# Performance work log

Hardware: AMD Instinct MI355X
Metric: run time of the kernel (lower is better)

Reference implementation:

```python
import jax, jax.numpy as jnp
import numpy as np

N_STROKES = 512
H = 256
W = 256
EPS = 1e-6


def setup_inputs() -> dict:
    key = jax.random.key(0)
    k1, k2, k3, k4, k5, k6 = jax.random.split(key, 6)
    canvas = jnp.zeros((3, H, W), dtype=jnp.float32)
    target = jax.random.uniform(k1, (3, H, W), dtype=jnp.float32)
    offset = jax.random.normal(k2, (N_STROKES, 2, 1), dtype=jnp.float32) * 0.5 + 0.5
    sigma = jax.random.uniform(k3, (N_STROKES, 2, 1), dtype=jnp.float32) * 0.5 + 0.2
    theta = jax.random.uniform(k4, (N_STROKES, 1), dtype=jnp.float32) * (2.0 * np.pi)
    color = jax.random.uniform(k5, (N_STROKES, 3, 1, 1), dtype=jnp.float32)
    alpha = jax.random.normal(k6, (N_STROKES, 1, 1, 1), dtype=jnp.float32) * 0.1
    return {"canvas": canvas, "target": target, "offset": offset,
            "sigma": sigma, "theta": theta, "color": color, "alpha": alpha}


def reference(canvas, target, offset, sigma, theta, color, alpha):
    h, w = canvas.shape[-2:]
    ratio = w / h  # width_to_height_ratio

    # normalized pixel grid, matching torch.linspace(0, w-1, w)/w
    ws = jnp.arange(w, dtype=jnp.float32) / w
    hs = jnp.arange(h, dtype=jnp.float32) / h
    x, y = jnp.meshgrid(ws, hs, indexing="xy")          # (H, W) each
    coords = jnp.stack([x, y], axis=0).reshape(1, 2, -1)  # (1, 2, H*W)
    coords = coords - offset                              # (n, 2, H*W)

    # rotation matrix per stroke: [[cos, -sin], [sin, -cos]] (as in source)
    cos_t = jnp.cos(theta)
    sin_t = jnp.sin(theta)
    rot = jnp.concatenate([cos_t, -sin_t, sin_t, -cos_t], axis=-1).reshape(-1, 2, 2)
    coords = jnp.einsum("nij,njp->nip", rot, coords)      # (n, 2, H*W)

    # aspect-corrected sigma (only for the gaussian field, not the loss)
    sig = jnp.concatenate([sigma[:, :1] / ratio, sigma[:, 1:]], axis=1)  # (n, 2, 1)

    quad = jnp.sum(jnp.square(coords) / (2.0 * jnp.square(sig)), axis=1)  # (n, H*W)
    pdf = jnp.exp(-quad)
    maxes = jnp.max(pdf, axis=-1, keepdims=True)          # per-stroke max-normalize
    pdf = pdf / (maxes + EPS)

    strokes = pdf.reshape(-1, 1, h, w) * alpha * color    # (n, 3, H, W)
    out = jax.nn.sigmoid(canvas + jnp.sum(strokes, axis=0))

    # loss_fn(out, target)
    l2 = jnp.mean(jnp.square(out - target))
    sharpness = jnp.mean(jnp.abs(1.0 - sigma[:, 0] / sigma[:, 1])) * 0.001
    transparency = -jnp.mean(jnp.abs(alpha)) * 0.001
    mse = jnp.mean(jnp.square(target - out))
    psnr = 10.0 * jnp.log10(1.0 / (mse + 1e-12))
    loss = l2 + transparency + sharpness - psnr / 30.0
    return out, loss
```

## Files before the change

kernel.cpp:

```cpp
#include <hip/hip_runtime.h>
#include <hip/hip_bf16.h>

#define HH 256
#define WW 256
#define NPIX (HH*WW)
#define NS 512

#define A_P  0
#define A_Q  1
#define A_T1 2
#define A_R  3
#define A_S  4
#define A_T2 5
#define A_C0 6
#define A_C1 7
#define A_C2 8
#define A_SH 9
#define A_TR 10
#define L2_SLOT  (11*NS)
#define CNT_SLOT (11*NS + 1)

#define TEAMS 8
#define SPT   (NS/TEAMS)
#define PPT   4
#define BLK   512
#define K2_GRID 256

#define L2E 1.4426950408889634f

#if __has_builtin(__builtin_amdgcn_exp2f)
#define EXP2F(x) __builtin_amdgcn_exp2f(x)
#else
#define EXP2F(x) exp2f(x)
#endif
#if __has_builtin(__builtin_amdgcn_rcpf)
#define RCPF(x) __builtin_amdgcn_rcpf(x)
#else
#define RCPF(x) (1.0f/(x))
#endif

__global__ __launch_bounds__(256) void k1_prep(
    const float* __restrict__ offset, const float* __restrict__ sigma,
    const float* __restrict__ theta,  const float* __restrict__ color,
    const float* __restrict__ alpha,  float* __restrict__ wsf)
{
    const int n = blockIdx.x;
    const int i = threadIdx.x;

    const float ox = offset[2*n], oy = offset[2*n+1];
    const float s0 = sigma[2*n],  s1 = sigma[2*n+1];
    const float th = theta[n];

    const float kk = sqrtf(0.5f * L2E);
    const float ra = kk / s0;
    const float rb = kk / s1;

    float s, c;
    __sincosf(th, &s, &c);
    const float P = ra * c,  Q = -ra * s,  T1 = ra * (-c * ox + s * oy);
    const float R = rb * s,  S = -rb * c,  T2 = rb * (-s * ox + c * oy);

    const float y     = (float)i / (float)HH;
    const float beta  = fmaf(Q, y, T1);
    const float delta = fmaf(S, y, T2);
    const float A     = P * P + R * R;
    const float xstar = -(P * beta + R * delta) / A;
    int j0 = (int)floorf(xstar * (float)WW);
    j0 = max(0, min(WW - 1, j0));
    const int j1 = min(WW - 1, j0 + 1);
    const float x0 = (float)j0 / (float)WW, x1 = (float)j1 / (float)WW;
    const float u0 = fmaf(P, x0, beta),  v0 = fmaf(R, x0, delta);
    const float u1 = fmaf(P, x1, beta),  v1 = fmaf(R, x1, delta);
    float q = fminf(u0*u0 + v0*v0, u1*u1 + v1*v1);

    #pragma unroll
    for (int off = 32; off > 0; off >>= 1)
        q = fminf(q, __shfl_down(q, off));
    __shared__ float wmin[4];
    if ((i & 63) == 0) wmin[i >> 6] = q;
    __syncthreads();

    if (i == 0) {
        const float qmin   = fminf(fminf(wmin[0], wmin[1]), fminf(wmin[2], wmin[3]));
        const float maxpdf = EXP2F(-qmin);
        const float base   = alpha[n] / (maxpdf + 1e-6f);
        wsf[A_P *NS + n] = P;
        wsf[A_Q *NS + n] = Q;
        wsf[A_T1*NS + n] = T1;
        wsf[A_R *NS + n] = R;
        wsf[A_S *NS + n] = S;
        wsf[A_T2*NS + n] = T2;
        wsf[A_C0*NS + n] = base * color[3*n];
        wsf[A_C1*NS + n] = base * color[3*n+1];
        wsf[A_C2*NS + n] = base * color[3*n+2];
        wsf[A_SH*NS + n] = fabsf(1.0f - s0 / s1);
        wsf[A_TR*NS + n] = fabsf(alpha[n]);
        if (n == 0) {
            wsf[L2_SLOT] = 0.0f;
            ((int*)wsf)[CNT_SLOT] = 0;
        }
    }
}

__global__ __launch_bounds__(512) void k2_paint(
    const float* __restrict__ canvas, const float* __restrict__ target,
    const float* __restrict__ prm,    float* __restrict__ out,
    float* __restrict__ l2acc,        int* __restrict__ cnt)
{
    const int tid  = threadIdx.x;
    const int t    = tid & 63;
    const int team = tid >> 6;
    const int row  = blockIdx.x;
    const float y  = (float)row * (1.0f / (float)HH);

    __shared__ float sprm[NS * 8];
    __shared__ float sacc[TEAMS][WW][3];

    {
        const int n = tid;
        const float P  = prm[A_P *NS + n];
        const float Q  = prm[A_Q *NS + n];
        const float T1 = prm[A_T1*NS + n];
        const float R  = prm[A_R *NS + n];
        const float S  = prm[A_S *NS + n];
        const float T2 = prm[A_T2*NS + n];
        const float c0 = prm[A_C0*NS + n];
        const float c1 = prm[A_C1*NS + n];
        const float c2 = prm[A_C2*NS + n];
        float4* sp4 = (float4*)(sprm + n * 8);
        sp4[0] = make_float4(P, R, fmaf(Q, y, T1), fmaf(S, y, T2));
        sp4[1] = make_float4(c0, c1, c2, 0.0f);
    }
    __syncthreads();

    float xk[PPT];
    #pragma unroll
    for (int k = 0; k < PPT; ++k) xk[k] = (float)(t + 64*k) * (1.0f / (float)WW);

    float acc[PPT][3] = {};
    const float4* __restrict__ tp4 = (const float4*)sprm + team * SPT * 2;

    #pragma unroll 4
    for (int n = 0; n < SPT; ++n) {
        const float4 g0 = tp4[2*n];
        const float4 g1 = tp4[2*n + 1];
        #pragma unroll
        for (int k = 0; k < PPT; ++k) {
            const float U = fmaf(g0.x, xk[k], g0.z);
            const float V = fmaf(g0.y, xk[k], g0.w);
            const float e = EXP2F(-fmaf(U, U, V * V));
            acc[k][0] = fmaf(e, g1.x, acc[k][0]);
            acc[k][1] = fmaf(e, g1.y, acc[k][1]);
            acc[k][2] = fmaf(e, g1.z, acc[k][2]);
        }
    }

    #pragma unroll
    for (int k = 0; k < PPT; ++k) {
        sacc[team][t + 64*k][0] = acc[k][0];
        sacc[team][t + 64*k][1] = acc[k][1];
        sacc[team][t + 64*k][2] = acc[k][2];
    }
    __syncthreads();

    __shared__ float lw[4];
    __shared__ int sdone;
    if (tid < WW) {
        float z0 = 0.0f, z1 = 0.0f, z2 = 0.0f;
        #pragma unroll
        for (int tm = 0; tm < TEAMS; ++tm) {
            z0 += sacc[tm][tid][0];
            z1 += sacc[tm][tid][1];
            z2 += sacc[tm][tid][2];
        }
        const int p = row * WW + tid;
        z0 += canvas[p];
        z1 += canvas[NPIX + p];
        z2 += canvas[2*NPIX + p];
        const float o0 = RCPF(1.0f + EXP2F(-z0 * L2E));
        const float o1 = RCPF(1.0f + EXP2F(-z1 * L2E));
        const float o2 = RCPF(1.0f + EXP2F(-z2 * L2E));
        out[p]          = o0;
        out[NPIX + p]   = o1;
        out[2*NPIX + p] = o2;
        const float d0 = o0 - target[p];
        const float d1 = o1 - target[NPIX + p];
        const float d2 = o2 - target[2*NPIX + p];
        float l2loc = d0*d0 + d1*d1 + d2*d2;
        #pragma unroll
        for (int off = 32; off > 0; off >>= 1)
            l2loc += __shfl_down(l2loc, off);
        if (t == 0) lw[tid >> 6] = l2loc;
    }
    __syncthreads();

    if (tid == 0) {
        atomicAdd(l2acc, lw[0] + lw[1] + lw[2] + lw[3]);
        __threadfence();
        const int old = atomicAdd(cnt, 1);
        sdone = (old == K2_GRID - 1) ? 1 : 0;
    }
    __syncthreads();

    if (sdone) {
        float sh = prm[A_SH*NS + tid];
        float tr = prm[A_TR*NS + tid];
        #pragma unroll
        for (int off = 32; off > 0; off >>= 1) {
            sh += __shfl_down(sh, off);
            tr += __shfl_down(tr, off);
        }
        if (t == 0) { sacc[0][team][0] = sh; sacc[0][team][1] = tr; }
        __syncthreads();
        if (tid == 0) {
            float shs = 0.0f, trs = 0.0f;
            #pragma unroll
            for (int w = 0; w < TEAMS; ++w) { shs += sacc[0][w][0]; trs += sacc[0][w][1]; }
            const float l2tot  = atomicAdd(l2acc, 0.0f);
            const float l2     = l2tot / (float)(3 * NPIX);
            const float sharp  = (shs / (float)NS) * 0.001f;
            const float transp = -(trs / (float)NS) * 0.001f;
            const float psnr   = 10.0f * log10f(1.0f / (l2 + 1e-12f));
            out[3 * NPIX] = l2 + transp + sharp - psnr / 30.0f;
        }
    }
}

extern "C" void kernel_launch(void* const* d_in, const int* in_sizes, int n_in,
                              void* d_out, int out_size, void* d_ws, size_t ws_size,
                              hipStream_t stream)
{
    const float* canvas = (const float*)d_in[0];
    const float* target = (const float*)d_in[1];
    const float* offset = (const float*)d_in[2];
    const float* sigma  = (const float*)d_in[3];
    const float* theta  = (const float*)d_in[4];
    const float* color  = (const float*)d_in[5];
    const float* alpha  = (const float*)d_in[6];
    float* out = (float*)d_out;
    float* wsf = (float*)d_ws;

    k1_prep<<<NS, 256, 0, stream>>>(offset, sigma, theta, color, alpha, wsf);
    k2_paint<<<K2_GRID, BLK, 0, stream>>>(canvas, target, wsf, out,
                                          wsf + L2_SLOT, (int*)wsf + CNT_SLOT);
}
```

Baseline: 86.86 us.

## Broadcast stroke params via readlane and double waves per block

Each wave now loads its own 32 strokes into lanes and broadcasts them with readlane (scalar registers), replacing the LDS staging buffer and its barrier. Block size grows to 1024 threads with 16 teams of 32 strokes each, which adds more waves per row and halves each wave's stroke loop. The costs are larger LDS for the partial sums (16x256x3 floats), a 16-way final reduction, and a fully unrolled loop that may raise register pressure.

```diff
diff --git a/kernel.cpp b/kernel.cpp
--- a/kernel.cpp
+++ b/kernel.cpp
@@ -20,10 +20,10 @@
 #define L2_SLOT  (11*NS)
 #define CNT_SLOT (11*NS + 1)
 
-#define TEAMS 8
+#define TEAMS 16
 #define SPT   (NS/TEAMS)
 #define PPT   4
-#define BLK   512
+#define BLK   1024
 #define K2_GRID 256
 
 #define L2E 1.4426950408889634f
@@ -38,6 +38,14 @@
 #else
 #define RCPF(x) (1.0f/(x))
 #endif
+
+__device__ __forceinline__ float rlane(float v, int l) {
+#if __has_builtin(__builtin_amdgcn_readlane)
+    return __int_as_float(__builtin_amdgcn_readlane(__float_as_int(v), l));
+#else
+    return __shfl(v, l, 64);
+#endif
+}
 
 __global__ __launch_bounds__(256) void k1_prep(
     const float* __restrict__ offset, const float* __restrict__ sigma,
@@ -102,64 +110,61 @@
     }
 }
 
-__global__ __launch_bounds__(512) void k2_paint(
+__global__ __launch_bounds__(1024) void k2_paint(
     const float* __restrict__ canvas, const float* __restrict__ target,
     const float* __restrict__ prm,    float* __restrict__ out,
     float* __restrict__ l2acc,        int* __restrict__ cnt)
 {
     const int tid  = threadIdx.x;
     const int t    = tid & 63;
-    const int team = tid >> 6;
+    const int w    = tid >> 6;
     const int row  = blockIdx.x;
     const float y  = (float)row * (1.0f / (float)HH);
 
-    __shared__ float sprm[NS * 8];
-    __shared__ float sacc[TEAMS][WW][3];
-
-    {
-        const int n = tid;
-        const float P  = prm[A_P *NS + n];
-        const float Q  = prm[A_Q *NS + n];
-        const float T1 = prm[A_T1*NS + n];
-        const float R  = prm[A_R *NS + n];
-        const float S  = prm[A_S *NS + n];
-        const float T2 = prm[A_T2*NS + n];
-        const float c0 = prm[A_C0*NS + n];
-        const float c1 = prm[A_C1*NS + n];
-        const float c2 = prm[A_C2*NS + n];
-        float4* sp4 = (float4*)(sprm + n * 8);
-        sp4[0] = make_float4(P, R, fmaf(Q, y, T1), fmaf(S, y, T2));
-        sp4[1] = make_float4(c0, c1, c2, 0.0f);
-    }
-    __syncthreads();
+    float rP = 0.0f, rR = 0.0f, rB = 0.0f, rD = 0.0f;
+    float rc0 = 0.0f, rc1 = 0.0f, rc2 = 0.0f;
+    if (t < SPT) {
+        const int n = w * SPT + t;
+        rP  = prm[A_P *NS + n];
+        rR  = prm[A_R *NS + n];
+        rB  = fmaf(prm[A_Q*NS + n], y, prm[A_T1*NS + n]);
+        rD  = fmaf(prm[A_S*NS + n], y, prm[A_T2*NS + n]);
+        rc0 = prm[A_C0*NS + n];
+        rc1 = prm[A_C1*NS + n];
+        rc2 = prm[A_C2*NS + n];
+    }
 
     float xk[PPT];
     #pragma unroll
     for (int k = 0; k < PPT; ++k) xk[k] = (float)(t + 64*k) * (1.0f / (float)WW);
 
     float acc[PPT][3] = {};
-    const float4* __restrict__ tp4 = (const float4*)sprm + team * SPT * 2;
-
-    #pragma unroll 4
+    #pragma unroll
     for (int n = 0; n < SPT; ++n) {
-        const float4 g0 = tp4[2*n];
-        const float4 g1 = tp4[2*n + 1];
+        const float P  = rlane(rP,  n);
+        const float R  = rlane(rR,  n);
+        const float B  = rlane(rB,  n);
+        const float D  = rlane(rD,  n);
+        const float c0 = rlane(rc0, n);
+        const float c1 = rlane(rc1, n);
+        const float c2 = rlane(rc2, n);
         #pragma unroll
         for (int k = 0; k < PPT; ++k) {
-            const float U = fmaf(g0.x, xk[k], g0.z);
-            const float V = fmaf(g0.y, xk[k], g0.w);
+            const float U = fmaf(P, xk[k], B);
+            const float V = fmaf(R, xk[k], D);
             const float e = EXP2F(-fmaf(U, U, V * V));
-            acc[k][0] = fmaf(e, g1.x, acc[k][0]);
-            acc[k][1] = fmaf(e, g1.y, acc[k][1]);
-            acc[k][2] = fmaf(e, g1.z, acc[k][2]);
-        }
-    }
-
+            acc[k][0] = fmaf(e, c0, acc[k][0]);
+            acc[k][1] = fmaf(e, c1, acc[k][1]);
+            acc[k][2] = fmaf(e, c2, acc[k][2]);
+        }
+    }
+
+    __shared__ float sacc[TEAMS][WW][3];
     #pragma unroll
     for (int k = 0; k < PPT; ++k) {
-        sacc[team][t + 64*k][0] = acc[k][0];
-        sacc[team][t + 64*k][1] = acc[k][1];
-        sacc[team][t + 64*k][2] = acc[k][2];
+        sacc[w][t + 64*k][0] = acc[k][0];
+        sacc[w][t + 64*k][1] = acc[k][1];
+        sacc[w][t + 64*k][2] = acc[k][2];
     }
     __syncthreads();
 
@@ -203,19 +208,21 @@
     __syncthreads();
 
     if (sdone) {
-        float sh = prm[A_SH*NS + tid];
-        float tr = prm[A_TR*NS + tid];
-        #pragma unroll
-        for (int off = 32; off > 0; off >>= 1) {
-            sh += __shfl_down(sh, off);
-            tr += __shfl_down(tr, off);
-        }
-        if (t == 0) { sacc[0][team][0] = sh; sacc[0][team][1] = tr; }
+        if (tid < NS) {
+            float sh = prm[A_SH*NS + tid];
+            float tr = prm[A_TR*NS + tid];
+            #pragma unroll
+            for (int off = 32; off > 0; off >>= 1) {
+                sh += __shfl_down(sh, off);
+                tr += __shfl_down(tr, off);
+            }
+            if (t == 0) { sacc[0][w][0] = sh; sacc[0][w][1] = tr; }
+        }
         __syncthreads();
         if (tid == 0) {
             float shs = 0.0f, trs = 0.0f;
             #pragma unroll
-            for (int w = 0; w < TEAMS; ++w) { shs += sacc[0][w][0]; trs += sacc[0][w][1]; }
+            for (int v = 0; v < NS/64; ++v) { shs += sacc[0][v][0]; trs += sacc[0][v][1]; }
             const float l2tot  = atomicAdd(l2acc, 0.0f);
             const float l2     = l2tot / (float)(3 * NPIX);
             const float sharp  = (shs / (float)NS) * 0.001f;
```

After: 86.24 us. No clear change (-0.7%).
